# Kernel optimization log

Hardware: AMD Instinct MI355X
Metric: run time of the kernel (lower is better)

## Reference

```python
import jax, jax.numpy as jnp
import numpy as np
import math

STAGE_NUM = 10
K = 8
C = 256
KAPPA = 20.0


def _l2norm(x, axis):
    return x / (1e-06 + jnp.linalg.norm(x, axis=axis, keepdims=True))


def setup_inputs() -> dict:
    key = jax.random.key(0)
    k1, k2 = jax.random.split(key)
    support_feature = jax.random.normal(k1, (16, C, 128, 128), dtype=jnp.float32)
    mu = jax.random.normal(k2, (1, C, K), dtype=jnp.float32) * math.sqrt(2.0 / K)
    mu = _l2norm(mu, axis=1)  # matches mu.normal_(0, sqrt(2/k)) then _l2norm(dim=1)
    return {"support_feature": support_feature, "mu": mu}


def _em(x, mu0):
    # x: [b, c, n]; mu0: [b, c, k]
    b, c, n = x.shape

    def step(i, carry):
        mu, _ = carry
        # Kernel: kappa * x^T @ mu -> [b, n, k]
        z = jax.nn.softmax(KAPPA * jnp.einsum('bcn,bck->bnk', x, mu), axis=2)
        z_ = z / (1e-06 + z.sum(axis=1, keepdims=True))  # normalize over n
        mu = jnp.einsum('bcn,bnk->bck', x, z_)           # mu update
        mu = _l2norm(mu, axis=1)
        return (mu, z_)

    z_init = jnp.zeros((b, n, K), dtype=x.dtype)
    mu, z_ = jax.lax.fori_loop(0, STAGE_NUM, step, (mu0, z_init))
    return mu.transpose(0, 2, 1), z_  # mu: [b, k, c]


def reference(support_feature, mu):
    b, c, h, w = support_feature.shape
    x = support_feature.reshape(b, c, h * w)
    mu_b = jnp.broadcast_to(mu, (b, c, K))
    # Original runs EM entirely under torch.no_grad()
    mu_f, z_ = jax.lax.stop_gradient(_em(x, mu_b))
    # prototypes in original are list of mu_f[:, i, :, None, None]; return stacked mu_f
    return (mu_f, z_)
```

## Files before the change

### kernel.cpp

```cpp
#include <hip/hip_runtime.h>
#include <cstdint>
#include <cstddef>

#define NB 16
#define NC 256
#define NK 8
#define NN 16384
#define NSTAGE 10
#define FKAPPA 20.0f

__global__ __launch_bounds__(256) void k_init_mu(const float* __restrict__ mu_in,
                                                 float* __restrict__ mu_cur) {
    int i = blockIdx.x * 256 + threadIdx.x;
    mu_cur[i] = mu_in[i & (NC * NK - 1)];
}

__global__ __launch_bounds__(256) void k_assign(const float* __restrict__ x,
                                                const float* __restrict__ mu,
                                                float* __restrict__ z,
                                                float* __restrict__ colsum) {
    const int b  = blockIdx.x >> 4;
    const int nt = blockIdx.x & 15;
    const int t  = threadIdx.x;

    __shared__ float smu[NC * NK];
    for (int i = t; i < NC * NK; i += 256) smu[i] = mu[b * NC * NK + i];
    __syncthreads();

    const int n0 = nt * 1024 + t * 4;
    const float* xp = x + (size_t)b * NC * NN + n0;

    float acc[4][NK];
    #pragma unroll
    for (int i = 0; i < 4; i++)
        #pragma unroll
        for (int k = 0; k < NK; k++) acc[i][k] = 0.f;

    #pragma unroll 4
    for (int c = 0; c < NC; c++) {
        const float4 xv = *reinterpret_cast<const float4*>(xp + (size_t)c * NN);
        const float4 m0 = *reinterpret_cast<const float4*>(&smu[c * NK]);
        const float4 m1 = *reinterpret_cast<const float4*>(&smu[c * NK + 4]);
        const float xs0 = xv.x, xs1 = xv.y, xs2 = xv.z, xs3 = xv.w;
        acc[0][0] += xs0 * m0.x; acc[0][1] += xs0 * m0.y; acc[0][2] += xs0 * m0.z; acc[0][3] += xs0 * m0.w;
        acc[0][4] += xs0 * m1.x; acc[0][5] += xs0 * m1.y; acc[0][6] += xs0 * m1.z; acc[0][7] += xs0 * m1.w;
        acc[1][0] += xs1 * m0.x; acc[1][1] += xs1 * m0.y; acc[1][2] += xs1 * m0.z; acc[1][3] += xs1 * m0.w;
        acc[1][4] += xs1 * m1.x; acc[1][5] += xs1 * m1.y; acc[1][6] += xs1 * m1.z; acc[1][7] += xs1 * m1.w;
        acc[2][0] += xs2 * m0.x; acc[2][1] += xs2 * m0.y; acc[2][2] += xs2 * m0.z; acc[2][3] += xs2 * m0.w;
        acc[2][4] += xs2 * m1.x; acc[2][5] += xs2 * m1.y; acc[2][6] += xs2 * m1.z; acc[2][7] += xs2 * m1.w;
        acc[3][0] += xs3 * m0.x; acc[3][1] += xs3 * m0.y; acc[3][2] += xs3 * m0.z; acc[3][3] += xs3 * m0.w;
        acc[3][4] += xs3 * m1.x; acc[3][5] += xs3 * m1.y; acc[3][6] += xs3 * m1.z; acc[3][7] += xs3 * m1.w;
    }

    float csum[NK];
    #pragma unroll
    for (int k = 0; k < NK; k++) csum[k] = 0.f;

    float* zp = z + ((size_t)b * NN + n0) * NK;
    #pragma unroll
    for (int i = 0; i < 4; i++) {
        float l[NK];
        float m = -1e30f;
        #pragma unroll
        for (int k = 0; k < NK; k++) { l[k] = FKAPPA * acc[i][k]; m = fmaxf(m, l[k]); }
        float s = 0.f;
        #pragma unroll
        for (int k = 0; k < NK; k++) { l[k] = __expf(l[k] - m); s += l[k]; }
        const float inv = 1.f / s;
        #pragma unroll
        for (int k = 0; k < NK; k++) { l[k] *= inv; csum[k] += l[k]; }
        *reinterpret_cast<float4*>(zp + i * NK)     = make_float4(l[0], l[1], l[2], l[3]);
        *reinterpret_cast<float4*>(zp + i * NK + 4) = make_float4(l[4], l[5], l[6], l[7]);
    }

    #pragma unroll
    for (int off = 32; off > 0; off >>= 1)
        #pragma unroll
        for (int k = 0; k < NK; k++) csum[k] += __shfl_down(csum[k], off, 64);

    __shared__ float red[4][NK];
    const int wave = t >> 6, lane = t & 63;
    if (lane == 0)
        #pragma unroll
        for (int k = 0; k < NK; k++) red[wave][k] = csum[k];
    __syncthreads();
    if (t < NK) {
        float s = red[0][t] + red[1][t] + red[2][t] + red[3][t];
        atomicAdd(&colsum[b * NK + t], s);
    }
}

__global__ __launch_bounds__(256) void k_update(const float* __restrict__ x,
                                                const float* __restrict__ z,
                                                const float* __restrict__ colsum,
                                                float* __restrict__ mu_out) {
    const int b  = blockIdx.x >> 5;
    const int ct = blockIdx.x & 31;
    const int c0 = ct * 8;
    const int t  = threadIdx.x;

    const float* xp = x + (size_t)b * NC * NN;
    const float* zp = z + (size_t)b * NN * NK;

    float acc[8][NK];
    #pragma unroll
    for (int ci = 0; ci < 8; ci++)
        #pragma unroll
        for (int k = 0; k < NK; k++) acc[ci][k] = 0.f;

    for (int it = 0; it < NN / 1024; ++it) {
        const int n0 = it * 1024 + t * 4;
        float zv[4][NK];
        #pragma unroll
        for (int i = 0; i < 4; i++) {
            const float4 z0 = *reinterpret_cast<const float4*>(zp + (size_t)(n0 + i) * NK);
            const float4 z1 = *reinterpret_cast<const float4*>(zp + (size_t)(n0 + i) * NK + 4);
            zv[i][0] = z0.x; zv[i][1] = z0.y; zv[i][2] = z0.z; zv[i][3] = z0.w;
            zv[i][4] = z1.x; zv[i][5] = z1.y; zv[i][6] = z1.z; zv[i][7] = z1.w;
        }
        #pragma unroll
        for (int ci = 0; ci < 8; ci++) {
            const float4 xv = *reinterpret_cast<const float4*>(xp + (size_t)(c0 + ci) * NN + n0);
            const float xs[4] = {xv.x, xv.y, xv.z, xv.w};
            #pragma unroll
            for (int i = 0; i < 4; i++)
                #pragma unroll
                for (int k = 0; k < NK; k++) acc[ci][k] += xs[i] * zv[i][k];
        }
    }

    #pragma unroll
    for (int off = 32; off > 0; off >>= 1)
        #pragma unroll
        for (int ci = 0; ci < 8; ci++)
            #pragma unroll
            for (int k = 0; k < NK; k++) acc[ci][k] += __shfl_down(acc[ci][k], off, 64);

    __shared__ float red[4][64];
    const int wave = t >> 6, lane = t & 63;
    if (lane == 0) {
        #pragma unroll
        for (int ci = 0; ci < 8; ci++)
            #pragma unroll
            for (int k = 0; k < NK; k++) red[wave][ci * NK + k] = acc[ci][k];
    }
    __syncthreads();
    if (t < 64) {
        const float s = red[0][t] + red[1][t] + red[2][t] + red[3][t];
        const int ci = t >> 3, k = t & 7;
        const float inv = 1.f / (1e-6f + colsum[b * NK + k]);
        mu_out[(size_t)b * NC * NK + (size_t)(c0 + ci) * NK + k] = s * inv;
    }
}

__global__ __launch_bounds__(256) void k_l2norm(const float* __restrict__ mu_in,
                                                float* __restrict__ mu_out) {
    const int b = blockIdx.x;
    const int t = threadIdx.x;
    const float4 v0 = *reinterpret_cast<const float4*>(mu_in + (size_t)b * NC * NK + t * NK);
    const float4 v1 = *reinterpret_cast<const float4*>(mu_in + (size_t)b * NC * NK + t * NK + 4);
    float v[NK] = {v0.x, v0.y, v0.z, v0.w, v1.x, v1.y, v1.z, v1.w};

    float sq[NK];
    #pragma unroll
    for (int k = 0; k < NK; k++) sq[k] = v[k] * v[k];
    #pragma unroll
    for (int off = 32; off > 0; off >>= 1)
        #pragma unroll
        for (int k = 0; k < NK; k++) sq[k] += __shfl_down(sq[k], off, 64);

    __shared__ float red[4][NK];
    const int wave = t >> 6, lane = t & 63;
    if (lane == 0)
        #pragma unroll
        for (int k = 0; k < NK; k++) red[wave][k] = sq[k];
    __syncthreads();
    __shared__ float scale[NK];
    if (t < NK) {
        const float tot = red[0][t] + red[1][t] + red[2][t] + red[3][t];
        scale[t] = 1.f / (1e-6f + sqrtf(tot));
    }
    __syncthreads();
    #pragma unroll
    for (int k = 0; k < NK; k++) v[k] *= scale[k];
    *reinterpret_cast<float4*>(mu_out + (size_t)b * NC * NK + t * NK)     = make_float4(v[0], v[1], v[2], v[3]);
    *reinterpret_cast<float4*>(mu_out + (size_t)b * NC * NK + t * NK + 4) = make_float4(v[4], v[5], v[6], v[7]);
}

__global__ __launch_bounds__(256) void k_write_mu(const float* __restrict__ mu,
                                                  float* __restrict__ out) {
    const int i = blockIdx.x * 256 + threadIdx.x;
    const int b = i >> 11, r = i & 2047;
    const int k = r >> 8, c = r & 255;
    out[i] = mu[(size_t)b * NC * NK + c * NK + k];
}

__global__ __launch_bounds__(256) void k_write_z(const float* __restrict__ z,
                                                 const float* __restrict__ colsum,
                                                 float* __restrict__ out) {
    const int i = blockIdx.x * 256 + threadIdx.x;
    const int b = i >> 14;
    float inv[NK];
    #pragma unroll
    for (int k = 0; k < NK; k++) inv[k] = 1.f / (1e-6f + colsum[b * NK + k]);
    const float4 z0 = *reinterpret_cast<const float4*>(z + (size_t)i * NK);
    const float4 z1 = *reinterpret_cast<const float4*>(z + (size_t)i * NK + 4);
    *reinterpret_cast<float4*>(out + (size_t)i * NK)     = make_float4(z0.x * inv[0], z0.y * inv[1], z0.z * inv[2], z0.w * inv[3]);
    *reinterpret_cast<float4*>(out + (size_t)i * NK + 4) = make_float4(z1.x * inv[4], z1.y * inv[5], z1.z * inv[6], z1.w * inv[7]);
}

extern "C" void kernel_launch(void* const* d_in, const int* in_sizes, int n_in,
                              void* d_out, int out_size, void* d_ws, size_t ws_size,
                              hipStream_t stream) {
    const float* x     = (const float*)d_in[0];
    const float* mu_in = (const float*)d_in[1];
    float* out = (float*)d_out;
    char* ws = (char*)d_ws;

    float* z      = (float*)ws;
    float* colsum = (float*)(ws + (size_t)NB * NN * NK * 4);
    float* mu_a   = (float*)(ws + (size_t)NB * NN * NK * 4 + 8192);
    float* mu_b   = (float*)(ws + (size_t)NB * NN * NK * 4 + 8192 + (size_t)NB * NC * NK * 4);

    hipMemsetAsync(colsum, 0, NSTAGE * NB * NK * sizeof(float), stream);
    k_init_mu<<<NB * NC * NK / 256, 256, 0, stream>>>(mu_in, mu_a);

    for (int s = 0; s < NSTAGE; ++s) {
        float* cs = colsum + s * NB * NK;
        k_assign<<<NB * 16, 256, 0, stream>>>(x, mu_a, z, cs);
        k_update<<<NB * 32, 256, 0, stream>>>(x, z, cs, mu_b);
        k_l2norm<<<NB, 256, 0, stream>>>(mu_b, mu_a);
    }

    k_write_mu<<<NB * NK * NC / 256, 256, 0, stream>>>(mu_a, out);
    k_write_z<<<NB * NN / 256, 256, 0, stream>>>(z, colsum + (NSTAGE - 1) * NB * NK,
                                                 out + NB * NK * NC);
}
```

Baseline: 1.410 ms.

## Fuse assignment and mu-update into one pass over x per stage

Merges the softmax assignment and the weighted-sum update into a single kernel. Each block loads a 64-column tile of x into shared memory, computes z for those columns, then accumulates the partial x·z into a per-stage numerator buffer through global atomics. The goal is to read x once per EM stage instead of twice. The cost is a large shared tile that limits occupancy and a large number of global atomic adds, and z is written only on the final stage.

```diff
diff --git a/kernel.cpp b/kernel.cpp
--- a/kernel.cpp
+++ b/kernel.cpp
@@ -15,151 +15,104 @@
     mu_cur[i] = mu_in[i & (NC * NK - 1)];
 }
 
-__global__ __launch_bounds__(256) void k_assign(const float* __restrict__ x,
-                                                const float* __restrict__ mu,
-                                                float* __restrict__ z,
-                                                float* __restrict__ colsum) {
-    const int b  = blockIdx.x >> 4;
-    const int nt = blockIdx.x & 15;
+template <bool WRITE_Z>
+__global__ __launch_bounds__(256) void k_stage(const float* __restrict__ x,
+                                               const float* __restrict__ mu,
+                                               float* __restrict__ num,
+                                               float* __restrict__ colsum,
+                                               float* __restrict__ zout) {
+    const int b  = blockIdx.x >> 8;
+    const int nt = blockIdx.x & 255;
     const int t  = threadIdx.x;
+    const int n  = t & 63;
+    const int p  = t >> 6;
 
-    __shared__ float smu[NC * NK];
+    __shared__ __align__(16) float xt[64][257];
+    __shared__ __align__(16) float smu[NC * NK];
+    __shared__ __align__(16) float dz[64][NK];
+
     for (int i = t; i < NC * NK; i += 256) smu[i] = mu[b * NC * NK + i];
+    if (t < 128) reinterpret_cast<float4*>(dz)[t] = make_float4(0.f, 0.f, 0.f, 0.f);
     __syncthreads();
 
-    const int n0 = nt * 1024 + t * 4;
-    const float* xp = x + (size_t)b * NC * NN + n0;
+    const int n0 = nt * 64;
+    const float* xp = x + (size_t)b * NC * NN + n0 + n;
 
-    float acc[4][NK];
+    float acc[NK];
     #pragma unroll
-    for (int i = 0; i < 4; i++)
-        #pragma unroll
-        for (int k = 0; k < NK; k++) acc[i][k] = 0.f;
+    for (int k = 0; k < NK; k++) acc[k] = 0.f;
 
-    #pragma unroll 4
-    for (int c = 0; c < NC; c++) {
-        const float4 xv = *reinterpret_cast<const float4*>(xp + (size_t)c * NN);
+    const int c0 = p * 64;
+    #pragma unroll 8
+    for (int ci = 0; ci < 64; ++ci) {
+        const int c = c0 + ci;
+        const float xv = xp[(size_t)c * NN];
+        xt[n][c] = xv;
         const float4 m0 = *reinterpret_cast<const float4*>(&smu[c * NK]);
         const float4 m1 = *reinterpret_cast<const float4*>(&smu[c * NK + 4]);
-        const float xs0 = xv.x, xs1 = xv.y, xs2 = xv.z, xs3 = xv.w;
-        acc[0][0] += xs0 * m0.x; acc[0][1] += xs0 * m0.y; acc[0][2] += xs0 * m0.z; acc[0][3] += xs0 * m0.w;
-        acc[0][4] += xs0 * m1.x; acc[0][5] += xs0 * m1.y; acc[0][6] += xs0 * m1.z; acc[0][7] += xs0 * m1.w;
-        acc[1][0] += xs1 * m0.x; acc[1][1] += xs1 * m0.y; acc[1][2] += xs1 * m0.z; acc[1][3] += xs1 * m0.w;
-        acc[1][4] += xs1 * m1.x; acc[1][5] += xs1 * m1.y; acc[1][6] += xs1 * m1.z; acc[1][7] += xs1 * m1.w;
-        acc[2][0] += xs2 * m0.x; acc[2][1] += xs2 * m0.y; acc[2][2] += xs2 * m0.z; acc[2][3] += xs2 * m0.w;
-        acc[2][4] += xs2 * m1.x; acc[2][5] += xs2 * m1.y; acc[2][6] += xs2 * m1.z; acc[2][7] += xs2 * m1.w;
-        acc[3][0] += xs3 * m0.x; acc[3][1] += xs3 * m0.y; acc[3][2] += xs3 * m0.z; acc[3][3] += xs3 * m0.w;
-        acc[3][4] += xs3 * m1.x; acc[3][5] += xs3 * m1.y; acc[3][6] += xs3 * m1.z; acc[3][7] += xs3 * m1.w;
+        acc[0] += xv * m0.x; acc[1] += xv * m0.y; acc[2] += xv * m0.z; acc[3] += xv * m0.w;
+        acc[4] += xv * m1.x; acc[5] += xv * m1.y; acc[6] += xv * m1.z; acc[7] += xv * m1.w;
     }
+    #pragma unroll
+    for (int k = 0; k < NK; k++) atomicAdd(&dz[n][k], acc[k]);
+    __syncthreads();
 
-    float csum[NK];
-    #pragma unroll
-    for (int k = 0; k < NK; k++) csum[k] = 0.f;
-
-    float* zp = z + ((size_t)b * NN + n0) * NK;
-    #pragma unroll
-    for (int i = 0; i < 4; i++) {
+    if (t < 64) {
         float l[NK];
         float m = -1e30f;
         #pragma unroll
-        for (int k = 0; k < NK; k++) { l[k] = FKAPPA * acc[i][k]; m = fmaxf(m, l[k]); }
+        for (int k = 0; k < NK; k++) { l[k] = FKAPPA * dz[t][k]; m = fmaxf(m, l[k]); }
         float s = 0.f;
         #pragma unroll
         for (int k = 0; k < NK; k++) { l[k] = __expf(l[k] - m); s += l[k]; }
         const float inv = 1.f / s;
         #pragma unroll
-        for (int k = 0; k < NK; k++) { l[k] *= inv; csum[k] += l[k]; }
-        *reinterpret_cast<float4*>(zp + i * NK)     = make_float4(l[0], l[1], l[2], l[3]);
-        *reinterpret_cast<float4*>(zp + i * NK + 4) = make_float4(l[4], l[5], l[6], l[7]);
+        for (int k = 0; k < NK; k++) { l[k] *= inv; dz[t][k] = l[k]; }
+        #pragma unroll
+        for (int off = 32; off > 0; off >>= 1)
+            #pragma unroll
+            for (int k = 0; k < NK; k++) l[k] += __shfl_down(l[k], off, 64);
+        if (t == 0)
+            #pragma unroll
+            for (int k = 0; k < NK; k++) atomicAdd(&colsum[b * NK + k], l[k]);
+    }
+    __syncthreads();
+
+    if (WRITE_Z) {
+        if (t < 128)
+            reinterpret_cast<float4*>(zout + ((size_t)b * NN + n0) * NK)[t] =
+                reinterpret_cast<const float4*>(dz)[t];
     }
 
+    float a2[NK];
     #pragma unroll
-    for (int off = 32; off > 0; off >>= 1)
-        #pragma unroll
-        for (int k = 0; k < NK; k++) csum[k] += __shfl_down(csum[k], off, 64);
-
-    __shared__ float red[4][NK];
-    const int wave = t >> 6, lane = t & 63;
-    if (lane == 0)
-        #pragma unroll
-        for (int k = 0; k < NK; k++) red[wave][k] = csum[k];
-    __syncthreads();
-    if (t < NK) {
-        float s = red[0][t] + red[1][t] + red[2][t] + red[3][t];
-        atomicAdd(&colsum[b * NK + t], s);
+    for (int k = 0; k < NK; k++) a2[k] = 0.f;
+    #pragma unroll 8
+    for (int nn = 0; nn < 64; ++nn) {
+        const float xv = xt[nn][t];
+        const float4 z0 = *reinterpret_cast<const float4*>(&dz[nn][0]);
+        const float4 z1 = *reinterpret_cast<const float4*>(&dz[nn][4]);
+        a2[0] += xv * z0.x; a2[1] += xv * z0.y; a2[2] += xv * z0.z; a2[3] += xv * z0.w;
+        a2[4] += xv * z1.x; a2[5] += xv * z1.y; a2[6] += xv * z1.z; a2[7] += xv * z1.w;
     }
+    float* np_ = num + (size_t)b * NC * NK + (size_t)t * NK;
+    #pragma unroll
+    for (int k = 0; k < NK; k++) atomicAdd(&np_[k], a2[k]);
 }
 
-__global__ __launch_bounds__(256) void k_update(const float* __restrict__ x,
-                                                const float* __restrict__ z,
-                                                const float* __restrict__ colsum,
-                                                float* __restrict__ mu_out) {
-    const int b  = blockIdx.x >> 5;
-    const int ct = blockIdx.x & 31;
-    const int c0 = ct * 8;
-    const int t  = threadIdx.x;
-
-    const float* xp = x + (size_t)b * NC * NN;
-    const float* zp = z + (size_t)b * NN * NK;
-
-    float acc[8][NK];
-    #pragma unroll
-    for (int ci = 0; ci < 8; ci++)
-        #pragma unroll
-        for (int k = 0; k < NK; k++) acc[ci][k] = 0.f;
-
-    for (int it = 0; it < NN / 1024; ++it) {
-        const int n0 = it * 1024 + t * 4;
-        float zv[4][NK];
-        #pragma unroll
-        for (int i = 0; i < 4; i++) {
-            const float4 z0 = *reinterpret_cast<const float4*>(zp + (size_t)(n0 + i) * NK);
-            const float4 z1 = *reinterpret_cast<const float4*>(zp + (size_t)(n0 + i) * NK + 4);
-            zv[i][0] = z0.x; zv[i][1] = z0.y; zv[i][2] = z0.z; zv[i][3] = z0.w;
-            zv[i][4] = z1.x; zv[i][5] = z1.y; zv[i][6] = z1.z; zv[i][7] = z1.w;
-        }
-        #pragma unroll
-        for (int ci = 0; ci < 8; ci++) {
-            const float4 xv = *reinterpret_cast<const float4*>(xp + (size_t)(c0 + ci) * NN + n0);
-            const float xs[4] = {xv.x, xv.y, xv.z, xv.w};
-            #pragma unroll
-            for (int i = 0; i < 4; i++)
-                #pragma unroll
-                for (int k = 0; k < NK; k++) acc[ci][k] += xs[i] * zv[i][k];
-        }
-    }
-
-    #pragma unroll
-    for (int off = 32; off > 0; off >>= 1)
-        #pragma unroll
-        for (int ci = 0; ci < 8; ci++)
-            #pragma unroll
-            for (int k = 0; k < NK; k++) acc[ci][k] += __shfl_down(acc[ci][k], off, 64);
-
-    __shared__ float red[4][64];
-    const int wave = t >> 6, lane = t & 63;
-    if (lane == 0) {
-        #pragma unroll
-        for (int ci = 0; ci < 8; ci++)
-            #pragma unroll
-            for (int k = 0; k < NK; k++) red[wave][ci * NK + k] = acc[ci][k];
-    }
-    __syncthreads();
-    if (t < 64) {
-        const float s = red[0][t] + red[1][t] + red[2][t] + red[3][t];
-        const int ci = t >> 3, k = t & 7;
-        const float inv = 1.f / (1e-6f + colsum[b * NK + k]);
-        mu_out[(size_t)b * NC * NK + (size_t)(c0 + ci) * NK + k] = s * inv;
-    }
-}
-
-__global__ __launch_bounds__(256) void k_l2norm(const float* __restrict__ mu_in,
-                                                float* __restrict__ mu_out) {
+__global__ __launch_bounds__(256) void k_newmu(const float* __restrict__ num,
+                                               const float* __restrict__ colsum,
+                                               float* __restrict__ mu_out) {
     const int b = blockIdx.x;
     const int t = threadIdx.x;
-    const float4 v0 = *reinterpret_cast<const float4*>(mu_in + (size_t)b * NC * NK + t * NK);
-    const float4 v1 = *reinterpret_cast<const float4*>(mu_in + (size_t)b * NC * NK + t * NK + 4);
-    float v[NK] = {v0.x, v0.y, v0.z, v0.w, v1.x, v1.y, v1.z, v1.w};
+    float inv[NK];
+    #pragma unroll
+    for (int k = 0; k < NK; k++) inv[k] = 1.f / (1e-6f + colsum[b * NK + k]);
+
+    const float4 v0 = *reinterpret_cast<const float4*>(num + (size_t)b * NC * NK + t * NK);
+    const float4 v1 = *reinterpret_cast<const float4*>(num + (size_t)b * NC * NK + t * NK + 4);
+    float v[NK] = {v0.x * inv[0], v0.y * inv[1], v0.z * inv[2], v0.w * inv[3],
+                   v1.x * inv[4], v1.y * inv[5], v1.z * inv[6], v1.w * inv[7]};
 
     float sq[NK];
     #pragma unroll
@@ -217,19 +170,26 @@
     float* out = (float*)d_out;
     char* ws = (char*)d_ws;
 
+    const size_t Z_BYTES   = (size_t)NB * NN * NK * 4;
+    const size_t CS_BYTES  = (size_t)NSTAGE * NB * NK * 4;
+    const size_t NUM_BYTES = (size_t)NSTAGE * NB * NC * NK * 4;
+
     float* z      = (float*)ws;
-    float* colsum = (float*)(ws + (size_t)NB * NN * NK * 4);
-    float* mu_a   = (float*)(ws + (size_t)NB * NN * NK * 4 + 8192);
-    float* mu_b   = (float*)(ws + (size_t)NB * NN * NK * 4 + 8192 + (size_t)NB * NC * NK * 4);
+    float* colsum = (float*)(ws + Z_BYTES);
+    float* num    = (float*)(ws + Z_BYTES + CS_BYTES);
+    float* mu_a   = (float*)(ws + Z_BYTES + CS_BYTES + NUM_BYTES);
 
-    hipMemsetAsync(colsum, 0, NSTAGE * NB * NK * sizeof(float), stream);
+    hipMemsetAsync(colsum, 0, CS_BYTES + NUM_BYTES, stream);
     k_init_mu<<<NB * NC * NK / 256, 256, 0, stream>>>(mu_in, mu_a);
 
     for (int s = 0; s < NSTAGE; ++s) {
         float* cs = colsum + s * NB * NK;
-        k_assign<<<NB * 16, 256, 0, stream>>>(x, mu_a, z, cs);
-        k_update<<<NB * 32, 256, 0, stream>>>(x, z, cs, mu_b);
-        k_l2norm<<<NB, 256, 0, stream>>>(mu_b, mu_a);
+        float* nm = num + (size_t)s * NB * NC * NK;
+        if (s == NSTAGE - 1)
+            k_stage<true><<<NB * 256, 256, 0, stream>>>(x, mu_a, nm, cs, z);
+        else
+            k_stage<false><<<NB * 256, 256, 0, stream>>>(x, mu_a, nm, cs, z);
+        k_newmu<<<NB, 256, 0, stream>>>(nm, cs, mu_a);
     }
 
     k_write_mu<<<NB * NK * NC / 256, 256, 0, stream>>>(mu_a, out);
```

Measured after the change: 4.995 ms. 3.54x slower.
